# Optimization experiments

Measured on AMD Instinct MI355X. Metric: run time of the kernel, lower is better.

The kernel has to match this reference:

```python
import jax, jax.numpy as jnp
import numpy as np

T, B, I, H = 512, 128, 256, 512


def setup_inputs() -> dict:
    key = jax.random.key(0)
    ks = jax.random.split(key, 7)
    s = 1.0 / np.sqrt(I + H)  # torch nn.Linear default init bound
    x = jax.random.normal(ks[0], (T, B, I), dtype=jnp.float32)
    Wz = jax.random.uniform(ks[1], (H, I + H), jnp.float32, -s, s)
    bz = jax.random.uniform(ks[2], (H,), jnp.float32, -s, s)
    Wr = jax.random.uniform(ks[3], (H, I + H), jnp.float32, -s, s)
    br = jax.random.uniform(ks[4], (H,), jnp.float32, -s, s)
    Wh = jax.random.uniform(ks[5], (H, I + H), jnp.float32, -s, s)
    bh = jax.random.uniform(ks[6], (H,), jnp.float32, -s, s)
    return {"x": x, "Wz": Wz, "bz": bz, "Wr": Wr, "br": br, "Wh": Wh, "bh": bh}


def reference(x, Wz, bz, Wr, br, Wh, bh):
    # x: [T, B, I]; h: [B, H]. Concat order is (h, xt), matching torch.cat((h, xt), dim=1).
    Bsz = x.shape[1]
    Hsz = Wz.shape[0]
    h0 = jnp.zeros((Bsz, Hsz), dtype=x.dtype)

    def step(h, xt):
        hx = jnp.concatenate([h, xt], axis=1)          # [B, H+I]
        z = jax.nn.sigmoid(hx @ Wz.T + bz)             # update gate
        r = jax.nn.sigmoid(hx @ Wr.T + br)             # reset gate
        cand = jnp.tanh(jnp.concatenate([r * h, xt], axis=1) @ Wh.T + bh)
        h_new = (1.0 - z) * h + z * cand
        return h_new, h_new

    h_last, output = jax.lax.scan(step, h0, x)         # output: [T, B, H]
    return output, h_last[None]                        # mirror (output, (h,)) with h: [1, B, H]
```

## Files before the change

### kernel.cpp

```cpp
#include <hip/hip_runtime.h>
#include <hip/hip_fp16.h>

typedef unsigned int uint32;
typedef unsigned long long uint64;
typedef __attribute__((ext_vector_type(8))) _Float16 half8;
typedef __attribute__((ext_vector_type(4))) float f32x4;

#define T_STEPS 512
#define BSZ 128
#define ISZ 256
#define HSZ 512
#define K1  768
#define NG  8
#define BG  16
#define GC  32
#define NC  16
#define LDK 776
#define LDA 264
#define FSTRIDE 16

#define LDS_X   0
#define LDS_WZ  8448
#define LDS_WR  33280
#define LDS_WH  58112
#define LDS_SC  82944
#define SMEM_BYTES 87552

#define AST(p, v) __hip_atomic_store((p), (v), __ATOMIC_RELAXED, __HIP_MEMORY_SCOPE_AGENT)
#define ALD(p)    __hip_atomic_load((p), __ATOMIC_RELAXED, __HIP_MEMORY_SCOPE_AGENT)

__device__ __forceinline__ float sigm(float x) {
  float e = __expf(-fabsf(x));
  float s = 1.f / (1.f + e);
  return x >= 0.f ? s : 1.f - s;
}
__device__ __forceinline__ float tanhx(float x) {
  float e = __expf(-2.f * fabsf(x));
  float t = (1.f - e) / (1.f + e);
  return x >= 0.f ? t : -t;
}
__device__ __forceinline__ uint32 f2x(float a, float b) {
  __half2 t = __floats2half2_rn(a, b);
  return *reinterpret_cast<uint32*>(&t);
}
#define MFMA(a, b, c) __builtin_amdgcn_mfma_f32_16x16x32_f16((a), (b), (c), 0, 0, 0)

union HF { uint64 u[2]; half8 h8; };

__global__ __launch_bounds__(256, 1)
void gru_persist(const float* __restrict__ x,
                 const float* __restrict__ Wz, const float* __restrict__ bz,
                 const float* __restrict__ Wr, const float* __restrict__ br,
                 const float* __restrict__ Wh, const float* __restrict__ bh,
                 float* __restrict__ out,
                 unsigned short* h_buf, unsigned short* rh_buf, uint32* flags)
{
  extern __shared__ char smem[];
  _Float16* X_l  = (_Float16*)(smem + LDS_X);
  _Float16* Wz_l = (_Float16*)(smem + LDS_WZ);
  _Float16* Wr_l = (_Float16*)(smem + LDS_WR);
  _Float16* Wh_l = (_Float16*)(smem + LDS_WH);
  float*    sc   = (float*)(smem + LDS_SC);

  const int tid  = threadIdx.x;
  const int g    = blockIdx.x & 7;
  const int rank = blockIdx.x >> 3;
  uint32* gf = flags + g * GC * FSTRIDE;
  unsigned short* hbG  = h_buf  + (size_t)g * BG * HSZ;
  unsigned short* rhbG = rh_buf + (size_t)g * BG * HSZ;

  {
    const int r  = tid & 15;
    const int ch = tid >> 4;
    for (int mi = 0; mi < 3; ++mi) {
      const float* Ws = (mi == 0) ? Wz : (mi == 1 ? Wr : Wh);
      _Float16*    Ld = (mi == 0) ? Wz_l : (mi == 1 ? Wr_l : Wh_l);
      const float4* s = (const float4*)(Ws + (size_t)(rank * NC + r) * K1 + ch * 48);
      uint4* d = (uint4*)(Ld + r * LDK + ch * 48);
      #pragma unroll
      for (int j = 0; j < 6; ++j) {
        float4 v0 = s[2 * j], v1 = s[2 * j + 1];
        d[j] = make_uint4(f2x(v0.x, v0.y), f2x(v0.z, v0.w),
                          f2x(v1.x, v1.y), f2x(v1.z, v1.w));
      }
    }
  }

  const int cl = tid & 15, bl = tid >> 4;
  const int bl2 = tid & 15, cl2 = tid >> 4;
  const int cg = rank * NC + cl;
  const int bg = g * BG + bl;
  const int bg2 = g * BG + bl2;
  const float bz_r = bz[cg], br_r = br[cg], bh_r = bh[cg];

  float h_reg = 0.f, zg = 0.f;

  const int wv = tid >> 6, lane = tid & 63;
  const int mrow = lane & 15, q = lane >> 4;
  const int scO = bl * 18 + cl;

  const uint64* hfb = (const uint64*)(hbG  + (size_t)mrow * HSZ + wv * 128 + q * 8);
  const uint64* rfb = (const uint64*)(rhbG + (size_t)mrow * HSZ + wv * 128 + q * 8);

  float4 px0, px1, px2, px3;
  {
    const float4* xs = (const float4*)(x + (size_t)bg2 * ISZ + cl2 * 16);
    px0 = xs[0]; px1 = xs[1]; px2 = xs[2]; px3 = xs[3];
    uint4* xd = (uint4*)(X_l + bl2 * LDA + cl2 * 16);
    xd[0] = make_uint4(f2x(px0.x, px0.y), f2x(px0.z, px0.w),
                       f2x(px1.x, px1.y), f2x(px1.z, px1.w));
    xd[1] = make_uint4(f2x(px2.x, px2.y), f2x(px2.z, px2.w),
                       f2x(px3.x, px3.y), f2x(px3.z, px3.w));
    const float4* xs1 = (const float4*)(x + ((size_t)1 * BSZ + bg2) * ISZ + cl2 * 16);
    px0 = xs1[0]; px1 = xs1[1]; px2 = xs1[2]; px3 = xs1[3];
  }
  __syncthreads();

  for (int t = 0; t < T_STEPS; ++t) {
    f32x4 accR = {0.f, 0.f, 0.f, 0.f};
    f32x4 accZ = {0.f, 0.f, 0.f, 0.f};
    f32x4 accC = {0.f, 0.f, 0.f, 0.f};
    {
      const int kbx = wv * 64;
      const half8* Ap  = (const half8*)(X_l  + mrow * LDA + kbx + q * 8);
      const half8* BpR = (const half8*)(Wr_l + mrow * LDK + HSZ + kbx + q * 8);
      const half8* BpZ = (const half8*)(Wz_l + mrow * LDK + HSZ + kbx + q * 8);
      const half8* BpC = (const half8*)(Wh_l + mrow * LDK + HSZ + kbx + q * 8);
      half8 a0 = Ap[0], a1 = Ap[4];
      accR = MFMA(a0, BpR[0], accR);
      accZ = MFMA(a0, BpZ[0], accZ);
      accC = MFMA(a0, BpC[0], accC);
      accR = MFMA(a1, BpR[4], accR);
      accZ = MFMA(a1, BpZ[4], accZ);
      accC = MFMA(a1, BpC[4], accC);
    }

    half8 br0, br1, br2, br3;
    {
      const half8* BpR = (const half8*)(Wr_l + mrow * LDK + wv * 128 + q * 8);
      br0 = BpR[0]; br1 = BpR[4]; br2 = BpR[8]; br3 = BpR[12];
    }

    if (tid < GC) {
      const uint32 need = (uint32)(2 * t);
      while (ALD(gf + tid * FSTRIDE) < need) {}
    }
    __syncthreads();

    HF fh0, fh1, fh2, fh3;
    {
      fh0.u[0] = ALD(hfb +  0); fh0.u[1] = ALD(hfb +  1);
      fh1.u[0] = ALD(hfb +  8); fh1.u[1] = ALD(hfb +  9);
      fh2.u[0] = ALD(hfb + 16); fh2.u[1] = ALD(hfb + 17);
      fh3.u[0] = ALD(hfb + 24); fh3.u[1] = ALD(hfb + 25);
      f32x4 aR1 = {0.f, 0.f, 0.f, 0.f};
      accR = MFMA(fh0.h8, br0, accR);
      aR1  = MFMA(fh1.h8, br1, aR1);
      accR = MFMA(fh2.h8, br2, accR);
      aR1  = MFMA(fh3.h8, br3, aR1);
      float* scw = sc + wv * 288;
      #pragma unroll
      for (int i = 0; i < 4; ++i) scw[(q * 4 + i) * 18 + mrow] = accR[i] + aR1[i];
    }
    __syncthreads();

    {
      float rp = sc[scO] + sc[288 + scO] + sc[576 + scO] + sc[864 + scO] + br_r;
      float rhv = sigm(rp) * h_reg;
      __half hh = __float2half(rhv);
      uint32 lo = (uint32)__half_as_ushort(hh);
      uint32 hi = (uint32)__shfl_down((int)lo, 1);
      if (!(tid & 1))
        AST((uint32*)(rhbG + bl * HSZ + rank * NC + cl), lo | (hi << 16));
    }
    asm volatile("s_waitcnt vmcnt(0)" ::: "memory");
    __syncthreads();
    if (tid == 0) AST(gf + rank * FSTRIDE, (uint32)(2 * t + 1));

    {
      const half8* BpZ = (const half8*)(Wz_l + mrow * LDK + wv * 128 + q * 8);
      accZ = MFMA(fh0.h8, BpZ[0], accZ);
      accZ = MFMA(fh1.h8, BpZ[4], accZ);
      accZ = MFMA(fh2.h8, BpZ[8], accZ);
      accZ = MFMA(fh3.h8, BpZ[12], accZ);
      float* scw = sc + wv * 288;
      #pragma unroll
      for (int i = 0; i < 4; ++i) scw[(q * 4 + i) * 18 + mrow] = accZ[i];
    }
    if (t + 1 < T_STEPS) {
      uint4* xd = (uint4*)(X_l + bl2 * LDA + cl2 * 16);
      xd[0] = make_uint4(f2x(px0.x, px0.y), f2x(px0.z, px0.w),
                         f2x(px1.x, px1.y), f2x(px1.z, px1.w));
      xd[1] = make_uint4(f2x(px2.x, px2.y), f2x(px2.z, px2.w),
                         f2x(px3.x, px3.y), f2x(px3.z, px3.w));
    }
    if (t + 2 < T_STEPS) {
      const float4* xs = (const float4*)(x + ((size_t)(t + 2) * BSZ + bg2) * ISZ + cl2 * 16);
      px0 = xs[0]; px1 = xs[1]; px2 = xs[2]; px3 = xs[3];
    }
    __syncthreads();

    {
      float zp = sc[scO] + sc[288 + scO] + sc[576 + scO] + sc[864 + scO] + bz_r;
      zg = sigm(zp);
    }
    half8 bc0, bc1, bc2, bc3;
    {
      const half8* BpC = (const half8*)(Wh_l + mrow * LDK + wv * 128 + q * 8);
      bc0 = BpC[0]; bc1 = BpC[4]; bc2 = BpC[8]; bc3 = BpC[12];
    }
    if (tid < GC) {
      const uint32 need = (uint32)(2 * t + 1);
      while (ALD(gf + tid * FSTRIDE) < need) {}
    }
    __syncthreads();

    {
      HF fc0, fc1, fc2, fc3;
      fc0.u[0] = ALD(rfb +  0); fc0.u[1] = ALD(rfb +  1);
      fc1.u[0] = ALD(rfb +  8); fc1.u[1] = ALD(rfb +  9);
      fc2.u[0] = ALD(rfb + 16); fc2.u[1] = ALD(rfb + 17);
      fc3.u[0] = ALD(rfb + 24); fc3.u[1] = ALD(rfb + 25);
      f32x4 aC1 = {0.f, 0.f, 0.f, 0.f};
      accC = MFMA(fc0.h8, bc0, accC);
      aC1  = MFMA(fc1.h8, bc1, aC1);
      accC = MFMA(fc2.h8, bc2, accC);
      aC1  = MFMA(fc3.h8, bc3, aC1);
      float* scw = sc + wv * 288;
      #pragma unroll
      for (int i = 0; i < 4; ++i) scw[(q * 4 + i) * 18 + mrow] = accC[i] + aC1[i];
    }
    __syncthreads();

    float hn;
    {
      float cp = sc[scO] + sc[288 + scO] + sc[576 + scO] + sc[864 + scO] + bh_r;
      float cand = tanhx(cp);
      hn = (1.f - zg) * h_reg + zg * cand;
      h_reg = hn;
      __half hh = __float2half(hn);
      uint32 lo = (uint32)__half_as_ushort(hh);
      uint32 hi = (uint32)__shfl_down((int)lo, 1);
      if (!(tid & 1))
        AST((uint32*)(hbG + bl * HSZ + rank * NC + cl), lo | (hi << 16));
    }
    asm volatile("s_waitcnt vmcnt(0)" ::: "memory");
    __syncthreads();
    if (tid == 0) AST(gf + rank * FSTRIDE, (uint32)(2 * t + 2));

    out[((size_t)t * BSZ + bg) * HSZ + cg] = hn;
    if (t == T_STEPS - 1)
      out[((size_t)T_STEPS * BSZ + bg) * HSZ + cg] = hn;
  }
}

extern "C" void kernel_launch(void* const* d_in, const int* in_sizes, int n_in,
                              void* d_out, int out_size, void* d_ws, size_t ws_size,
                              hipStream_t stream) {
  const float* x  = (const float*)d_in[0];
  const float* Wz = (const float*)d_in[1];
  const float* bz = (const float*)d_in[2];
  const float* Wr = (const float*)d_in[3];
  const float* br = (const float*)d_in[4];
  const float* Wh = (const float*)d_in[5];
  const float* bh = (const float*)d_in[6];
  float* out = (float*)d_out;

  uint32* flags = (uint32*)d_ws;
  unsigned short* h_buf  = (unsigned short*)((char*)d_ws + NG * GC * FSTRIDE * 4);
  unsigned short* rh_buf = h_buf + NG * BG * HSZ;

  hipMemsetAsync(d_ws, 0, NG * GC * FSTRIDE * 4 + (size_t)NG * BG * HSZ * 2, stream);

  hipFuncSetAttribute(reinterpret_cast<const void*>(gru_persist),
                      hipFuncAttributeMaxDynamicSharedMemorySize, SMEM_BYTES);

  hipLaunchKernelGGL(gru_persist, dim3(NG * GC), dim3(256), SMEM_BYTES, stream,
                     x, Wz, bz, Wr, br, Wh, bh, out, h_buf, rh_buf, flags);
}
```

Before: 2.771 ms.

## Use per-wave flags and direct polling to cut block barriers in GRU step

Each wavefront now publishes its own progress flag and polls exactly the producer waves whose h/rh slices it reads, replacing the tid<32 spin followed by __syncthreads. The scratch buffer is split into three separate regions (r, z, candidate), so the z-gate reduction can be deferred into the final phase and one more block barrier can be removed. This is meant to shorten the serial critical path of each timestep by dropping several block-wide barriers. In exchange every lane spins on four flags, which adds polling traffic to global memory, and LDS use grows.

```diff
diff --git a/kernel.cpp b/kernel.cpp
--- a/kernel.cpp
+++ b/kernel.cpp
@@ -17,14 +17,15 @@
 #define NC  16
 #define LDK 776
 #define LDA 264
-#define FSTRIDE 16
+
+#define FLAG_U32_PER_RANK 16
 
 #define LDS_X   0
 #define LDS_WZ  8448
 #define LDS_WR  33280
 #define LDS_WH  58112
 #define LDS_SC  82944
-#define SMEM_BYTES 87552
+#define SMEM_BYTES 96768
 
 #define AST(p, v) __hip_atomic_store((p), (v), __ATOMIC_RELAXED, __HIP_MEMORY_SCOPE_AGENT)
 #define ALD(p)    __hip_atomic_load((p), __ATOMIC_RELAXED, __HIP_MEMORY_SCOPE_AGENT)
@@ -43,6 +44,7 @@
   __half2 t = __floats2half2_rn(a, b);
   return *reinterpret_cast<uint32*>(&t);
 }
+__device__ __forceinline__ uint32 umin2(uint32 a, uint32 b) { return a < b ? a : b; }
 #define MFMA(a, b, c) __builtin_amdgcn_mfma_f32_16x16x32_f16((a), (b), (c), 0, 0, 0)
 
 union HF { uint64 u[2]; half8 h8; };
@@ -60,12 +62,14 @@
   _Float16* Wz_l = (_Float16*)(smem + LDS_WZ);
   _Float16* Wr_l = (_Float16*)(smem + LDS_WR);
   _Float16* Wh_l = (_Float16*)(smem + LDS_WH);
-  float*    sc   = (float*)(smem + LDS_SC);
+  float*    scA  = (float*)(smem + LDS_SC);
+  float*    scB  = scA + 1152;
+  float*    scC  = scA + 2304;
 
   const int tid  = threadIdx.x;
   const int g    = blockIdx.x & 7;
   const int rank = blockIdx.x >> 3;
-  uint32* gf = flags + g * GC * FSTRIDE;
+  uint32* gf = flags + (size_t)g * GC * FLAG_U32_PER_RANK;
   unsigned short* hbG  = h_buf  + (size_t)g * BG * HSZ;
   unsigned short* rhbG = rh_buf + (size_t)g * BG * HSZ;
 
@@ -93,7 +97,7 @@
   const int bg2 = g * BG + bl2;
   const float bz_r = bz[cg], br_r = br[cg], bh_r = bh[cg];
 
-  float h_reg = 0.f, zg = 0.f;
+  float h_reg = 0.f;
 
   const int wv = tid >> 6, lane = tid & 63;
   const int mrow = lane & 15, q = lane >> 4;
@@ -101,6 +105,8 @@
 
   const uint64* hfb = (const uint64*)(hbG  + (size_t)mrow * HSZ + wv * 128 + q * 8);
   const uint64* rfb = (const uint64*)(rhbG + (size_t)mrow * HSZ + wv * 128 + q * 8);
+  const uint32* pfl = gf + (size_t)(8 * wv + (q >> 1)) * FLAG_U32_PER_RANK + (mrow >> 2);
+  uint32* myflag = gf + (size_t)rank * FLAG_U32_PER_RANK + wv;
 
   float4 px0, px1, px2, px3;
   {
@@ -141,12 +147,13 @@
       br0 = BpR[0]; br1 = BpR[4]; br2 = BpR[8]; br3 = BpR[12];
     }
 
-    if (tid < GC) {
+    {
       const uint32 need = (uint32)(2 * t);
-      while (ALD(gf + tid * FSTRIDE) < need) {}
-    }
-    __syncthreads();
-
+      while (true) {
+        uint32 v0 = ALD(pfl), v1 = ALD(pfl + 32), v2 = ALD(pfl + 64), v3 = ALD(pfl + 96);
+        if (umin2(umin2(v0, v1), umin2(v2, v3)) >= need) break;
+      }
+    }
     HF fh0, fh1, fh2, fh3;
     {
       fh0.u[0] = ALD(hfb +  0); fh0.u[1] = ALD(hfb +  1);
@@ -158,14 +165,14 @@
       aR1  = MFMA(fh1.h8, br1, aR1);
       accR = MFMA(fh2.h8, br2, accR);
       aR1  = MFMA(fh3.h8, br3, aR1);
-      float* scw = sc + wv * 288;
+      float* scw = scA + wv * 288;
       #pragma unroll
       for (int i = 0; i < 4; ++i) scw[(q * 4 + i) * 18 + mrow] = accR[i] + aR1[i];
     }
     __syncthreads();
 
     {
-      float rp = sc[scO] + sc[288 + scO] + sc[576 + scO] + sc[864 + scO] + br_r;
+      float rp = scA[scO] + scA[288 + scO] + scA[576 + scO] + scA[864 + scO] + br_r;
       float rhv = sigm(rp) * h_reg;
       __half hh = __float2half(rhv);
       uint32 lo = (uint32)__half_as_ushort(hh);
@@ -174,8 +181,7 @@
         AST((uint32*)(rhbG + bl * HSZ + rank * NC + cl), lo | (hi << 16));
     }
     asm volatile("s_waitcnt vmcnt(0)" ::: "memory");
-    __syncthreads();
-    if (tid == 0) AST(gf + rank * FSTRIDE, (uint32)(2 * t + 1));
+    if (lane == 0) AST(myflag, (uint32)(2 * t + 1));
 
     {
       const half8* BpZ = (const half8*)(Wz_l + mrow * LDK + wv * 128 + q * 8);
@@ -183,7 +189,7 @@
       accZ = MFMA(fh1.h8, BpZ[4], accZ);
       accZ = MFMA(fh2.h8, BpZ[8], accZ);
       accZ = MFMA(fh3.h8, BpZ[12], accZ);
-      float* scw = sc + wv * 288;
+      float* scw = scB + wv * 288;
       #pragma unroll
       for (int i = 0; i < 4; ++i) scw[(q * 4 + i) * 18 + mrow] = accZ[i];
     }
@@ -198,23 +204,20 @@
       const float4* xs = (const float4*)(x + ((size_t)(t + 2) * BSZ + bg2) * ISZ + cl2 * 16);
       px0 = xs[0]; px1 = xs[1]; px2 = xs[2]; px3 = xs[3];
     }
-    __syncthreads();
-
-    {
-      float zp = sc[scO] + sc[288 + scO] + sc[576 + scO] + sc[864 + scO] + bz_r;
-      zg = sigm(zp);
-    }
+
     half8 bc0, bc1, bc2, bc3;
     {
       const half8* BpC = (const half8*)(Wh_l + mrow * LDK + wv * 128 + q * 8);
       bc0 = BpC[0]; bc1 = BpC[4]; bc2 = BpC[8]; bc3 = BpC[12];
     }
-    if (tid < GC) {
+
+    {
       const uint32 need = (uint32)(2 * t + 1);
-      while (ALD(gf + tid * FSTRIDE) < need) {}
-    }
-    __syncthreads();
-
+      while (true) {
+        uint32 v0 = ALD(pfl), v1 = ALD(pfl + 32), v2 = ALD(pfl + 64), v3 = ALD(pfl + 96);
+        if (umin2(umin2(v0, v1), umin2(v2, v3)) >= need) break;
+      }
+    }
     {
       HF fc0, fc1, fc2, fc3;
       fc0.u[0] = ALD(rfb +  0); fc0.u[1] = ALD(rfb +  1);
@@ -226,7 +229,7 @@
       aC1  = MFMA(fc1.h8, bc1, aC1);
       accC = MFMA(fc2.h8, bc2, accC);
       aC1  = MFMA(fc3.h8, bc3, aC1);
-      float* scw = sc + wv * 288;
+      float* scw = scC + wv * 288;
       #pragma unroll
       for (int i = 0; i < 4; ++i) scw[(q * 4 + i) * 18 + mrow] = accC[i] + aC1[i];
     }
@@ -234,7 +237,9 @@
 
     float hn;
     {
-      float cp = sc[scO] + sc[288 + scO] + sc[576 + scO] + sc[864 + scO] + bh_r;
+      float zp = scB[scO] + scB[288 + scO] + scB[576 + scO] + scB[864 + scO] + bz_r;
+      float zg = sigm(zp);
+      float cp = scC[scO] + scC[288 + scO] + scC[576 + scO] + scC[864 + scO] + bh_r;
       float cand = tanhx(cp);
       hn = (1.f - zg) * h_reg + zg * cand;
       h_reg = hn;
@@ -245,8 +250,7 @@
         AST((uint32*)(hbG + bl * HSZ + rank * NC + cl), lo | (hi << 16));
     }
     asm volatile("s_waitcnt vmcnt(0)" ::: "memory");
-    __syncthreads();
-    if (tid == 0) AST(gf + rank * FSTRIDE, (uint32)(2 * t + 2));
+    if (lane == 0) AST(myflag, (uint32)(2 * t + 2));
 
     out[((size_t)t * BSZ + bg) * HSZ + cg] = hn;
     if (t == T_STEPS - 1)
@@ -267,10 +271,10 @@
   float* out = (float*)d_out;
 
   uint32* flags = (uint32*)d_ws;
-  unsigned short* h_buf  = (unsigned short*)((char*)d_ws + NG * GC * FSTRIDE * 4);
+  unsigned short* h_buf  = (unsigned short*)((char*)d_ws + NG * GC * FLAG_U32_PER_RANK * 4);
   unsigned short* rh_buf = h_buf + NG * BG * HSZ;
 
-  hipMemsetAsync(d_ws, 0, NG * GC * FSTRIDE * 4 + (size_t)NG * BG * HSZ * 2, stream);
+  hipMemsetAsync(d_ws, 0, NG * GC * FLAG_U32_PER_RANK * 4 + (size_t)NG * BG * HSZ * 2, stream);
 
   hipFuncSetAttribute(reinterpret_cast<const void*>(gru_persist),
                       hipFuncAttributeMaxDynamicSharedMemorySize, SMEM_BYTES);
```

Result: slower. 2.996 ms (+8.1%).
